# Kernel tuning notes

Hardware: AMD Instinct MI355X
Metric: run time of the kernel (lower is better)

Reference implementation:

```python
import jax, jax.numpy as jnp
import numpy as np


def _causal_kernel_mask(K):
    # casual_mask[i, K-i:] = 0 for i in 1..p
    p = K // 2
    m = np.ones((p + 1, K), np.float32)
    for i in range(1, p + 1):
        m[i, K - i:] = 0.0
    return jnp.asarray(m)


def setup_inputs() -> dict:
    rng = jax.random.key(0)
    k0, k1, k2, k3, k4 = jax.random.split(rng, 5)
    B, H, N, F = 2, 16, 1024, 64
    V, K = 32000, 5
    return {
        "input_ids": jax.random.randint(k0, (B, N), 0, V),
        "query": jax.random.normal(k1, (B, H, N, F), dtype=jnp.float32),
        "key": jax.random.normal(k2, (B, H, N, F), dtype=jnp.float32),
        "value": jax.random.normal(k3, (B, H, N, F), dtype=jnp.float32),
        "emb_weight": jax.random.normal(k4, (V, 2 * K), dtype=jnp.float32) * 0.02,
    }


def reference(input_ids, query, key, value, emb_weight):
    B, H, N, F = query.shape
    K = emb_weight.shape[1] // 2  # head/layer invariant -> emb dim = 2*K
    p = K // 2
    G = 2 * H

    # ---- get_kernel (layer 0; head_invariant + layer_invariant) ----
    kern = emb_weight[input_ids]                       # [B,N,2K]
    kern = kern.reshape(B, N, 2, 1, K)                 # [B,N,2,1,K]
    kern = jnp.broadcast_to(kern, (B, N, 2, H, K)).reshape(B, N, G, K)

    # ---- conv_key_value (for_casual=True, strict_on_casual=True) ----
    kv = jnp.concatenate([key, value], axis=1)         # [B,2H,N,F]
    kv_pad = jnp.pad(kv, ((0, 0), (0, 0), (p, p), (0, 0)))
    # unfold over token dim: [B,2H,K,N,F]
    kv_unf = jnp.stack([kv_pad[:, :, k:k + N, :] for k in range(K)], axis=2)
    cmask = _causal_kernel_mask(K)                     # [p+1,K]
    kern_m = kern[:, :, :, None, :] * cmask[None, None, None]  # [B,N,2H,p+1,K]
    # dynamic depthwise conv with per-offset causal masking
    out = jnp.einsum('bgknf,bngjk->bgjnf', kv_unf, kern_m)     # [B,2H,p+1,N,F]
    key_c = out[:, :H, 0]                              # [B,H,N,F]
    value_c = out[:, H:, 0]                            # [B,H,N,F]

    # ---- attention with causal-boundary corrections (n_past = 0) ----
    scale = 1.0 / jnp.sqrt(jnp.asarray(F, dtype=query.dtype))
    q = query * scale
    scores = jnp.einsum('bhnf,bhmf->bhnm', q, key_c)   # [B,H,N,N]

    # correct_attn_weights_near_casual_boundary
    for i in range(p):
        off = p - 1 - i
        cb_key = out[:, :H, 1 + i]                     # [B,H,N,F]
        corr = jnp.einsum('bhnf,bhnf->bhn', q[:, :, off:, :], cb_key[:, :, :N - off, :])
        rows = jnp.arange(N - off) + off
        cols = jnp.arange(N - off)
        scores = scores.at[:, :, rows, cols].set(corr)

    causal = jnp.tril(jnp.ones((N, N), dtype=bool))
    scores = jnp.where(causal, scores, jnp.asarray(-1e9, dtype=scores.dtype))
    probs = jax.nn.softmax(scores, axis=-1)
    attn = jnp.einsum('bhnm,bhmf->bhnf', probs, value_c)

    # correct_attn_output_near_casual_boundary
    for i in range(p):
        off = p - 1 - i
        cb_value = out[:, H:, 1 + i]                   # [B,H,N,F]
        idx = jnp.arange(N - off)
        diag_w = probs[:, :, idx + off, idx]           # diag offset=-off: [B,H,N-off]
        diff_v = cb_value[:, :, :N - off, :] - value_c[:, :, :N - off, :]
        diff = diag_w[..., None] * diff_v
        attn = attn + jnp.pad(diff, ((0, 0), (0, 0), (off, 0), (0, 0)))

    return attn
```

## Files before the change

kernel.cpp:

```cpp
#include <hip/hip_runtime.h>

#define HD    64
#define NSEQ  1024
#define NSLOT 40
#define CROWS 32
#define LOG2E 1.44269504088896f

typedef __attribute__((ext_vector_type(8))) __bf16 bf16x8;
typedef __attribute__((ext_vector_type(4))) float  f32x4;
typedef __attribute__((ext_vector_type(4))) unsigned short u16x4;

__device__ __constant__ unsigned char PAIRS[NSLOT] = {
    60,61,62,63, 56,57,58, 52,53,54, 48,49,50, 44,45,46,
    40,41, 36,37, 32,33, 28,29, 24, 20, 16, 12,
    59, 42, 25, 8, 55, 38, 21, 4, 51, 34, 17, 0 };

__device__ inline unsigned short f2bf(float x) {
    unsigned u = __float_as_uint(x);
    return (unsigned short)((u + 0x7fffu + ((u >> 16) & 1u)) >> 16);
}
__device__ inline unsigned pk2(float a, float b) {
    return (unsigned)f2bf(a) | ((unsigned)f2bf(b) << 16);
}
__device__ inline float bf2f(unsigned short s) {
    return __uint_as_float(((unsigned)s) << 16);
}
__device__ inline float dot4(f32x4 a, f32x4 b) {
    return a.x * b.x + a.y * b.y + a.z * b.z + a.w * b.w;
}

__global__ __launch_bounds__(256) void conv_kernel(
    const int* __restrict__ ids,
    const float* __restrict__ keyg,
    const float* __restrict__ valg,
    const float* __restrict__ qg,
    const float* __restrict__ emb,
    unsigned short* __restrict__ kc,
    unsigned short* __restrict__ vcT,
    float* __restrict__ dg1, float* __restrict__ dg2)
{
    __shared__ float se[(CROWS + 1) * 10];
    __shared__ float vtile[CROWS][68];
    int pid = blockIdx.x;
    int bh = pid & 31;
    int n0 = (pid >> 5) * CROWS;
    int b  = bh >> 4;
    int t  = threadIdx.x;
    size_t hb = (size_t)bh * NSEQ * HD;

    for (int u = t; u < (CROWS + 1) * 10; u += 256) {
        int r = u / 10, c = u - r * 10;
        int n = n0 - 1 + r;
        se[u] = (n >= 0) ? emb[(size_t)ids[b * NSEQ + n] * 10 + c] : 0.f;
    }
    __syncthreads();

    const float* kb = keyg + hb;
    const float* vb = valg + hb;
#pragma unroll
    for (int i = 0; i < 2; ++i) {
        int u  = (i << 8) + t;
        int nl = u >> 4, g4 = u & 15;
        int n  = n0 + nl, f = g4 << 2;
        const float* e  = se + (nl + 1) * 10;
        const float* ep = se + nl * 10;
        f32x4 xk[5], xv[5];
#pragma unroll
        for (int k = 0; k < 5; ++k) {
            int m = n + k - 2;
            if (m >= 0 && m < NSEQ) {
                xk[k] = *(const f32x4*)(kb + (size_t)m * HD + f);
                xv[k] = *(const f32x4*)(vb + (size_t)m * HD + f);
            } else {
                xk[k] = (f32x4){0.f, 0.f, 0.f, 0.f};
                xv[k] = (f32x4){0.f, 0.f, 0.f, 0.f};
            }
        }
        f32x4 km3 = (n >= 3) ? *(const f32x4*)(kb + (size_t)(n - 3) * HD + f)
                             : (f32x4){0.f, 0.f, 0.f, 0.f};
        f32x4 qv = *(const f32x4*)(qg + hb + (size_t)n * HD + f) * (0.125f * LOG2E);

        f32x4 k012 = e[0] * xk[0] + e[1] * xk[1] + e[2] * xk[2];
        f32x4 kcv  = k012 + e[3] * xk[3] + e[4] * xk[4];
        f32x4 vcv  = e[5] * xv[0] + e[6] * xv[1] + e[7] * xv[2] + e[8] * xv[3] + e[9] * xv[4];

        u16x4 kq;
        kq.x = f2bf(kcv.x); kq.y = f2bf(kcv.y); kq.z = f2bf(kcv.z); kq.w = f2bf(kcv.w);
        *(u16x4*)(kc + hb + (size_t)n * HD + f) = kq;
        *(f32x4*)(&vtile[nl][f]) = vcv;

        float s2 = dot4(qv, k012);
        f32x4 kj1 = ep[0] * km3 + ep[1] * xk[0] + ep[2] * xk[1] + ep[3] * xk[2];
        float s1 = dot4(qv, kj1);
#pragma unroll
        for (int o = 1; o < 16; o <<= 1) {
            s2 += __shfl_xor(s2, o, 64);
            s1 += __shfl_xor(s1, o, 64);
        }
        if (g4 == 0) {
            dg2[bh * NSEQ + n] = s2;
            dg1[bh * NSEQ + n] = s1;
        }
    }
    __syncthreads();
#pragma unroll
    for (int i = 0; i < 2; ++i) {
        int u = (i << 8) + t;
        int f = u >> 3, nn = (u & 7) << 2;
        u16x4 o;
        o.x = f2bf(vtile[nn + 0][f]);
        o.y = f2bf(vtile[nn + 1][f]);
        o.z = f2bf(vtile[nn + 2][f]);
        o.w = f2bf(vtile[nn + 3][f]);
        *(u16x4*)(vcT + ((size_t)bh * HD + f) * NSEQ + n0 + nn) = o;
    }
}

__global__ __launch_bounds__(256) void attn_kernel(
    const float* __restrict__ qg,
    const unsigned short* __restrict__ kc,
    const unsigned short* __restrict__ vcT,
    const float* __restrict__ dg1, const float* __restrict__ dg2,
    const float* __restrict__ valg, const int* __restrict__ ids,
    const float* __restrict__ emb,
    float* __restrict__ pML, unsigned short* __restrict__ pO,
    float* __restrict__ outg)
{
    __shared__ __align__(16) unsigned char sK[8192];
    __shared__ __align__(16) unsigned char sV[8192];
    __shared__ __align__(16) unsigned char sP[8192];

    int pid  = blockIdx.x;
    int bh   = pid & 31;
    int slot = pid >> 5;
    int code = PAIRS[slot];
    int j = code >> 2, cch = code & 3;
    int q0 = j << 6;
    int t0 = cch << 2;
    int len = j - (cch << 2) + 1; if (len > 4) len = 4;
    int nc  = (j >> 2) + 1;

    int t = threadIdx.x;
    int w = t >> 6, l = t & 63;
    int lq = l & 15, h = l >> 4, l7 = l & 7;
    int lid = h * 16 + lq;
    int qbw = q0 + w * 16;
    size_t hb = (size_t)bh * NSEQ * HD;

    const unsigned short* kcb = kc  + hb;
    const unsigned short* vtb = vcT + (size_t)bh * HD * NSEQ;

    bf16x8 qb0, qb1;
    {
        const float* qr = qg + hb + (size_t)(qbw + lq) * HD + 8 * h;
        f32x4 a0 = *(const f32x4*)(qr);
        f32x4 a1 = *(const f32x4*)(qr + 4);
        f32x4 b0 = *(const f32x4*)(qr + 32);
        f32x4 b1 = *(const f32x4*)(qr + 36);
        const float S = 0.125f * LOG2E;
        union { unsigned u[4]; bf16x8 v; } u0, u1;
        u0.u[0] = pk2(a0.x * S, a0.y * S); u0.u[1] = pk2(a0.z * S, a0.w * S);
        u0.u[2] = pk2(a1.x * S, a1.y * S); u0.u[3] = pk2(a1.z * S, a1.w * S);
        u1.u[0] = pk2(b0.x * S, b0.y * S); u1.u[1] = pk2(b0.z * S, b0.w * S);
        u1.u[2] = pk2(b1.x * S, b1.y * S); u1.u[3] = pk2(b1.z * S, b1.w * S);
        qb0 = u0.v; qb1 = u1.v;
    }
    float diag2_l = dg2[bh * NSEQ + qbw + lq];
    float diag1_l = dg1[bh * NSEQ + qbw + lq];

    f32x4 of[4];
#pragma unroll
    for (int ft = 0; ft < 4; ++ft) of[ft] = (f32x4){0.f, 0.f, 0.f, 0.f};
    float m_run = -1e30f, denom = 0.f;

    const int ka_off0 = ((0 + h) ^ l7) << 4;
    const int ka_off1 = ((4 + h) ^ l7) << 4;
    const int pr_base = w * 2048 + lq * 128;
    const int chk0 = ((qbw > 0 ? qbw - 1 : 0) >> 6);

    uint4 pf[4];
    auto issue = [&](int tg) {
        int kv0 = tg << 6;
#pragma unroll
        for (int i = 0; i < 4; ++i) {
            int chunk = t + (i << 8);
            int buf = chunk >> 9, loc = chunk & 511;
            int r = loc >> 3, c = loc & 7;
            int cs = c ^ (r & 7);
            pf[i] = (buf == 0)
                ? *(const uint4*)(kcb + (size_t)(kv0 + r) * HD + cs * 8)
                : *(const uint4*)(vtb + (size_t)r * NSEQ + kv0 + cs * 8);
        }
    };
    auto commit = [&]() {
#pragma unroll
        for (int i = 0; i < 4; ++i) {
            int chunk = t + (i << 8);
            int buf = chunk >> 9, loc = chunk & 511;
            int r = loc >> 3, c = loc & 7;
            *(uint4*)((buf ? sV : sK) + r * 128 + c * 16) = pf[i];
        }
    };

    issue(t0); commit();
    for (int ti = 0; ti < len; ++ti) {
        __syncthreads();
        if (ti + 1 < len) issue(t0 + ti + 1);
        int tg  = t0 + ti;
        int kv0 = tg << 6;

        f32x4 p[4];
#pragma unroll
        for (int st = 0; st < 4; ++st) {
            bf16x8 ka0 = *(const bf16x8*)(sK + st * 2048 + lq * 128 + ka_off0);
            bf16x8 ka1 = *(const bf16x8*)(sK + st * 2048 + lq * 128 + ka_off1);
            f32x4 d = (f32x4){0.f, 0.f, 0.f, 0.f};
            d = __builtin_amdgcn_mfma_f32_16x16x32_bf16(ka0, qb0, d, 0, 0, 0);
            d = __builtin_amdgcn_mfma_f32_16x16x32_bf16(ka1, qb1, d, 0, 0, 0);
            p[st] = d;
        }

        if (tg >= chk0) {
            int n_l = qbw + lq;
#pragma unroll
            for (int st = 0; st < 4; ++st)
#pragma unroll
                for (int r = 0; r < 4; ++r) {
                    int kv = kv0 + st * 16 + 4 * h + r;
                    float dd = p[st][r];
                    if (kv > n_l)           dd = -1e30f;
                    else if (kv == n_l)     dd = diag2_l;
                    else if (kv == n_l - 1) dd = diag1_l;
                    p[st][r] = dd;
                }
        }

        float tmax = -1e30f;
#pragma unroll
        for (int st = 0; st < 4; ++st)
#pragma unroll
            for (int r = 0; r < 4; ++r) tmax = fmaxf(tmax, p[st][r]);
        tmax = fmaxf(tmax, __shfl_xor(tmax, 16, 64));
        tmax = fmaxf(tmax, __shfl_xor(tmax, 32, 64));
        if (!__all(tmax <= m_run + 7.0f)) {
            float m_new = fmaxf(m_run, tmax);
            float alpha = __builtin_exp2f(m_run - m_new);
            denom *= alpha;
            m_run = m_new;
#pragma unroll
            for (int r = 0; r < 4; ++r) {
                float ar = __shfl(alpha, 4 * h + r, 64);
                of[0][r] *= ar; of[1][r] *= ar; of[2][r] *= ar; of[3][r] *= ar;
            }
        }
        float lsum = 0.f;
#pragma unroll
        for (int st = 0; st < 4; ++st)
#pragma unroll
            for (int r = 0; r < 4; ++r) {
                float e = __builtin_exp2f(p[st][r] - m_run);
                p[st][r] = e;
                lsum += e;
            }
        lsum += __shfl_xor(lsum, 16, 64);
        lsum += __shfl_xor(lsum, 32, 64);
        denom += lsum;

#pragma unroll
        for (int st = 0; st < 4; ++st) {
            uint2 uu;
            uu.x = pk2(p[st][0], p[st][1]);
            uu.y = pk2(p[st][2], p[st][3]);
            int chunk = (st << 1) + (h >> 1);
            *(uint2*)(sP + pr_base + ((chunk ^ l7) << 4) + ((h & 1) << 3)) = uu;
        }
        asm volatile("s_waitcnt lgkmcnt(0)" ::: "memory");
        __builtin_amdgcn_sched_barrier(0);

#pragma unroll
        for (int kk = 0; kk < 2; ++kk) {
            int koff = kk ? ka_off1 : ka_off0;
            bf16x8 pa = *(const bf16x8*)(sP + pr_base + koff);
#pragma unroll
            for (int ft = 0; ft < 4; ++ft) {
                bf16x8 vb = *(const bf16x8*)(sV + ft * 2048 + lq * 128 + koff);
                of[ft] = __builtin_amdgcn_mfma_f32_16x16x32_bf16(pa, vb, of[ft], 0, 0, 0);
            }
        }
        __syncthreads();
        if (ti + 1 < len) commit();
    }

    int psBase = ((bh << 4) | j) << 2;
    if (nc > 1) {
        if (h == 0) {
            float2 ml; ml.x = m_run; ml.y = denom;
            *(float2*)(pML + ((size_t)(psBase + cch) * 64 + w * 16 + lq) * 2) = ml;
        }
#pragma unroll
        for (int ft = 0; ft < 4; ++ft)
#pragma unroll
            for (int r = 0; r < 4; ++r)
                pO[(size_t)((((psBase + cch) * 4 + w) * 4 + ft) * 4 + r) * 64 + lid] =
                    f2bf(of[ft][r]);
        return;
    }

    const float* vraw = valg + hb;
    float* outr = outg + hb;
    const int* idb = ids + (size_t)(bh >> 4) * NSEQ;
#pragma unroll
    for (int r = 0; r < 4; ++r) {
        int qrow = 4 * h + r;
        int n = qbw + qrow;
        float dn = __shfl(denom,   qrow, 64);
        float mf = __shfl(m_run,   qrow, 64);
        float d2 = __shfl(diag2_l, qrow, 64);
        float d1 = __shfl(diag1_l, qrow, 64);
        float inv = 1.0f / dn;
        float p2 = __builtin_exp2f(d2 - mf) * inv;
        float p1 = (n >= 1) ? __builtin_exp2f(d1 - mf) * inv : 0.f;
        int id_n = idb[n];
        float e8  = emb[(size_t)id_n * 10 + 8];
        float e9  = emb[(size_t)id_n * 10 + 9];
        float e9p = (n >= 1) ? emb[(size_t)idb[n - 1] * 10 + 9] : 0.f;
        float ca = -(p2 * e8 + p1 * e9p);
        float cb = -p2 * e9;
#pragma unroll
        for (int ft = 0; ft < 4; ++ft) {
            int f = ft * 16 + lq;
            float v = of[ft][r] * inv;
            if (n + 1 < NSEQ) v += ca * vraw[(size_t)(n + 1) * HD + f];
            if (n + 2 < NSEQ) v += cb * vraw[(size_t)(n + 2) * HD + f];
            outr[(size_t)n * HD + f] = v;
        }
    }
}

__global__ __launch_bounds__(256) void merge_kernel(
    const float* __restrict__ pML, const unsigned short* __restrict__ pO,
    const float* __restrict__ dg1, const float* __restrict__ dg2,
    const float* __restrict__ valg, const int* __restrict__ ids,
    const float* __restrict__ emb, float* __restrict__ outg)
{
    int pid = blockIdx.x;
    int bh = pid & 31, j = (pid >> 5) + 4;
    int nc = (j >> 2) + 1;
    int t = threadIdx.x;
    int rloc = t >> 2, fg = t & 3;
    int n = (j << 6) + rloc;
    int f0 = fg << 4;
    size_t hb = (size_t)bh * NSEQ * HD;
    int psBase = ((bh << 4) | j) << 2;

    float mc[4], lc[4];
    float mg = -3e30f;
    for (int c = 0; c < nc; ++c) {
        float2 v = *(const float2*)(pML + ((size_t)(psBase + c) * 64 + rloc) * 2);
        mc[c] = v.x; lc[c] = v.y;
        mg = fmaxf(mg, mc[c]);
    }
    float D = 0.f;
    f32x4 a0 = (f32x4){0.f,0.f,0.f,0.f}, a1 = a0, a2 = a0, a3 = a0;
    for (int c = 0; c < nc; ++c) {
        float wc = __builtin_exp2f(mc[c] - mg);
        D += lc[c] * wc;
        const unsigned short* pp = pO +
            (size_t)((((psBase + c) * 4 + (rloc >> 4)) * 4 + fg) * 4 + (rloc & 3)) * 64
            + ((rloc >> 2) & 3) * 16;
        uint4 ua = *(const uint4*)(pp);
        uint4 ub = *(const uint4*)(pp + 8);
        a0.x += wc * __uint_as_float(ua.x << 16);
        a0.y += wc * __uint_as_float(ua.x & 0xffff0000u);
        a0.z += wc * __uint_as_float(ua.y << 16);
        a0.w += wc * __uint_as_float(ua.y & 0xffff0000u);
        a1.x += wc * __uint_as_float(ua.z << 16);
        a1.y += wc * __uint_as_float(ua.z & 0xffff0000u);
        a1.z += wc * __uint_as_float(ua.w << 16);
        a1.w += wc * __uint_as_float(ua.w & 0xffff0000u);
        a2.x += wc * __uint_as_float(ub.x << 16);
        a2.y += wc * __uint_as_float(ub.x & 0xffff0000u);
        a2.z += wc * __uint_as_float(ub.y << 16);
        a2.w += wc * __uint_as_float(ub.y & 0xffff0000u);
        a3.x += wc * __uint_as_float(ub.z << 16);
        a3.y += wc * __uint_as_float(ub.z & 0xffff0000u);
        a3.z += wc * __uint_as_float(ub.w << 16);
        a3.w += wc * __uint_as_float(ub.w & 0xffff0000u);
    }
    float inv = 1.0f / D;
    float d2 = dg2[bh * NSEQ + n], d1 = dg1[bh * NSEQ + n];
    float p2 = __builtin_exp2f(d2 - mg) * inv;
    float p1 = (n >= 1) ? __builtin_exp2f(d1 - mg) * inv : 0.f;
    const int* idb = ids + (size_t)(bh >> 4) * NSEQ;
    int id_n = idb[n];
    float e8  = emb[(size_t)id_n * 10 + 8];
    float e9  = emb[(size_t)id_n * 10 + 9];
    float e9p = (n >= 1) ? emb[(size_t)idb[n - 1] * 10 + 9] : 0.f;
    float ca = -(p2 * e8 + p1 * e9p);
    float cb = -p2 * e9;

    a0 *= inv; a1 *= inv; a2 *= inv; a3 *= inv;
    if (n + 1 < NSEQ) {
        const float* v1 = valg + hb + (size_t)(n + 1) * HD + f0;
        a0 += ca * *(const f32x4*)(v1);
        a1 += ca * *(const f32x4*)(v1 + 4);
        a2 += ca * *(const f32x4*)(v1 + 8);
        a3 += ca * *(const f32x4*)(v1 + 12);
    }
    if (n + 2 < NSEQ) {
        const float* v2 = valg + hb + (size_t)(n + 2) * HD + f0;
        a0 += cb * *(const f32x4*)(v2);
        a1 += cb * *(const f32x4*)(v2 + 4);
        a2 += cb * *(const f32x4*)(v2 + 8);
        a3 += cb * *(const f32x4*)(v2 + 12);
    }
    float* o = outg + hb + (size_t)n * HD + f0;
    *(f32x4*)(o)      = a0;
    *(f32x4*)(o + 4)  = a1;
    *(f32x4*)(o + 8)  = a2;
    *(f32x4*)(o + 12) = a3;
}

extern "C" void kernel_launch(void* const* d_in, const int* in_sizes, int n_in,
                              void* d_out, int out_size, void* d_ws, size_t ws_size,
                              hipStream_t stream)
{
    const int*   ids = (const int*)  d_in[0];
    const float* q   = (const float*)d_in[1];
    const float* key = (const float*)d_in[2];
    const float* val = (const float*)d_in[3];
    const float* emb = (const float*)d_in[4];
    float* out = (float*)d_out;

    char* w = (char*)d_ws;
    unsigned short* kc  = (unsigned short*)(w);
    unsigned short* vcT = (unsigned short*)(w + (4u << 20));
    float* dg1 = (float*)(w + 8388608);
    float* dg2 = (float*)(w + 8519680);
    float* pML = (float*)(w + 8650752);
    unsigned short* pO = (unsigned short*)(w + 9699328);

    conv_kernel<<<1024, 256, 0, stream>>>(ids, key, val, q, emb, kc, vcT, dg1, dg2);
    attn_kernel<<<32 * NSLOT, 256, 0, stream>>>(q, kc, vcT, dg1, dg2, val, ids, emb,
                                                pML, pO, out);
    merge_kernel<<<384, 256, 0, stream>>>(pML, pO, dg1, dg2, val, ids, emb, out);
}
```

Baseline: 60.97 us.

## Split attention blocks into single-wave blocks loading K/V directly from global

The attention kernel is relaunched with one 64-thread wavefront per block, four times as many blocks, each owning one 16-row query slice. The shared-memory K/V staging, prefetch pipeline and block-wide barriers are removed, and each wave now reads its K and transposed-V fragments directly from global memory into registers. This aims to cut barrier stalls and LDS traffic and to raise occupancy, but each wave reloads the same K/V tiles its sibling waves used to share, which increases global/L2 traffic and leaves loads without an explicit prefetch.

```diff
diff --git a/kernel.cpp b/kernel.cpp
--- a/kernel.cpp
+++ b/kernel.cpp
@@ -21,9 +21,6 @@
 }
 __device__ inline unsigned pk2(float a, float b) {
     return (unsigned)f2bf(a) | ((unsigned)f2bf(b) << 16);
-}
-__device__ inline float bf2f(unsigned short s) {
-    return __uint_as_float(((unsigned)s) << 16);
 }
 __device__ inline float dot4(f32x4 a, f32x4 b) {
     return a.x * b.x + a.y * b.y + a.z * b.z + a.w * b.w;
@@ -116,7 +113,7 @@
     }
 }
 
-__global__ __launch_bounds__(256) void attn_kernel(
+__global__ __launch_bounds__(64, 4) void attn_kernel(
     const float* __restrict__ qg,
     const unsigned short* __restrict__ kc,
     const unsigned short* __restrict__ vcT,
@@ -126,13 +123,13 @@
     float* __restrict__ pML, unsigned short* __restrict__ pO,
     float* __restrict__ outg)
 {
-    __shared__ __align__(16) unsigned char sK[8192];
-    __shared__ __align__(16) unsigned char sV[8192];
-    __shared__ __align__(16) unsigned char sP[8192];
+    __shared__ __align__(16) unsigned char sP[2048];
 
     int pid  = blockIdx.x;
     int bh   = pid & 31;
-    int slot = pid >> 5;
+    int rest = pid >> 5;
+    int w    = rest & 3;
+    int slot = rest >> 2;
     int code = PAIRS[slot];
     int j = code >> 2, cch = code & 3;
     int q0 = j << 6;
@@ -140,8 +137,7 @@
     int len = j - (cch << 2) + 1; if (len > 4) len = 4;
     int nc  = (j >> 2) + 1;
 
-    int t = threadIdx.x;
-    int w = t >> 6, l = t & 63;
+    int l = threadIdx.x & 63;
     int lq = l & 15, h = l >> 4, l7 = l & 7;
     int lid = h * 16 + lq;
     int qbw = q0 + w * 16;
@@ -173,52 +169,37 @@
     for (int ft = 0; ft < 4; ++ft) of[ft] = (f32x4){0.f, 0.f, 0.f, 0.f};
     float m_run = -1e30f, denom = 0.f;
 
-    const int ka_off0 = ((0 + h) ^ l7) << 4;
-    const int ka_off1 = ((4 + h) ^ l7) << 4;
-    const int pr_base = w * 2048 + lq * 128;
+    const int pr_base = lq * 128;
     const int chk0 = ((qbw > 0 ? qbw - 1 : 0) >> 6);
 
-    uint4 pf[4];
-    auto issue = [&](int tg) {
-        int kv0 = tg << 6;
-#pragma unroll
-        for (int i = 0; i < 4; ++i) {
-            int chunk = t + (i << 8);
-            int buf = chunk >> 9, loc = chunk & 511;
-            int r = loc >> 3, c = loc & 7;
-            int cs = c ^ (r & 7);
-            pf[i] = (buf == 0)
-                ? *(const uint4*)(kcb + (size_t)(kv0 + r) * HD + cs * 8)
-                : *(const uint4*)(vtb + (size_t)r * NSEQ + kv0 + cs * 8);
-        }
-    };
-    auto commit = [&]() {
-#pragma unroll
-        for (int i = 0; i < 4; ++i) {
-            int chunk = t + (i << 8);
-            int buf = chunk >> 9, loc = chunk & 511;
-            int r = loc >> 3, c = loc & 7;
-            *(uint4*)((buf ? sV : sK) + r * 128 + c * 16) = pf[i];
-        }
-    };
-
-    issue(t0); commit();
     for (int ti = 0; ti < len; ++ti) {
-        __syncthreads();
-        if (ti + 1 < len) issue(t0 + ti + 1);
         int tg  = t0 + ti;
         int kv0 = tg << 6;
 
+        bf16x8 ka0[4], ka1[4];
+#pragma unroll
+        for (int st = 0; st < 4; ++st) {
+            const unsigned short* kr = kcb + (size_t)(kv0 + st * 16 + lq) * HD + 8 * h;
+            ka0[st] = *(const bf16x8*)(kr);
+            ka1[st] = *(const bf16x8*)(kr + 32);
+        }
+
         f32x4 p[4];
 #pragma unroll
         for (int st = 0; st < 4; ++st) {
-            bf16x8 ka0 = *(const bf16x8*)(sK + st * 2048 + lq * 128 + ka_off0);
-            bf16x8 ka1 = *(const bf16x8*)(sK + st * 2048 + lq * 128 + ka_off1);
             f32x4 d = (f32x4){0.f, 0.f, 0.f, 0.f};
-            d = __builtin_amdgcn_mfma_f32_16x16x32_bf16(ka0, qb0, d, 0, 0, 0);
-            d = __builtin_amdgcn_mfma_f32_16x16x32_bf16(ka1, qb1, d, 0, 0, 0);
+            d = __builtin_amdgcn_mfma_f32_16x16x32_bf16(ka0[st], qb0, d, 0, 0, 0);
+            d = __builtin_amdgcn_mfma_f32_16x16x32_bf16(ka1[st], qb1, d, 0, 0, 0);
             p[st] = d;
         }
+
+        bf16x8 vbv[2][4];
+#pragma unroll
+        for (int kk = 0; kk < 2; ++kk)
+#pragma unroll
+            for (int ft = 0; ft < 4; ++ft)
+                vbv[kk][ft] = *(const bf16x8*)(
+                    vtb + (size_t)(ft * 16 + lq) * NSEQ + kv0 + 8 * (4 * kk + h));
 
         if (tg >= chk0) {
             int n_l = qbw + lq;
@@ -279,16 +260,11 @@
 
 #pragma unroll
         for (int kk = 0; kk < 2; ++kk) {
-            int koff = kk ? ka_off1 : ka_off0;
-            bf16x8 pa = *(const bf16x8*)(sP + pr_base + koff);
-#pragma unroll
-            for (int ft = 0; ft < 4; ++ft) {
-                bf16x8 vb = *(const bf16x8*)(sV + ft * 2048 + lq * 128 + koff);
-                of[ft] = __builtin_amdgcn_mfma_f32_16x16x32_bf16(pa, vb, of[ft], 0, 0, 0);
-            }
-        }
-        __syncthreads();
-        if (ti + 1 < len) commit();
+            bf16x8 pa = *(const bf16x8*)(sP + pr_base + ((((kk << 2) + h) ^ l7) << 4));
+#pragma unroll
+            for (int ft = 0; ft < 4; ++ft)
+                of[ft] = __builtin_amdgcn_mfma_f32_16x16x32_bf16(pa, vbv[kk][ft], of[ft], 0, 0, 0);
+        }
     }
 
     int psBase = ((bh << 4) | j) << 2;
@@ -441,7 +417,7 @@
     unsigned short* pO = (unsigned short*)(w + 9699328);
 
     conv_kernel<<<1024, 256, 0, stream>>>(ids, key, val, q, emb, kc, vcT, dg1, dg2);
-    attn_kernel<<<32 * NSLOT, 256, 0, stream>>>(q, kc, vcT, dg1, dg2, val, ids, emb,
-                                                pML, pO, out);
+    attn_kernel<<<32 * NSLOT * 4, 64, 0, stream>>>(q, kc, vcT, dg1, dg2, val, ids, emb,
+                                                   pML, pO, out);
     merge_kernel<<<384, 256, 0, stream>>>(pML, pO, dg1, dg2, val, ids, emb, out);
 }
```

Result: slower. 71.89 us (+17.9%).

## Pair two query blocks per 512-thread workgroup sharing K/V tiles

Applied to the files above, without the earlier changes.

The attention kernel now processes two adjacent 64-row query blocks per workgroup (8 waves, 512 threads), so each K/V tile loaded into shared memory is reused by both blocks. This halves K/V global loads per query row and the grid shrinks from 40 to 20 slots per head. Waves whose query block does not need a tile skip compute but still hit the barriers. This adds some idle-wave imbalance, doubles the P scratch in LDS, and reduces the number of workgroups available to fill the GPU.

```diff
diff --git a/kernel.cpp b/kernel.cpp
--- a/kernel.cpp
+++ b/kernel.cpp
@@ -2,7 +2,7 @@
 
 #define HD    64
 #define NSEQ  1024
-#define NSLOT 40
+#define NPB   20
 #define CROWS 32
 #define LOG2E 1.44269504088896f
 
@@ -10,10 +10,9 @@
 typedef __attribute__((ext_vector_type(4))) float  f32x4;
 typedef __attribute__((ext_vector_type(4))) unsigned short u16x4;
 
-__device__ __constant__ unsigned char PAIRS[NSLOT] = {
-    60,61,62,63, 56,57,58, 52,53,54, 48,49,50, 44,45,46,
-    40,41, 36,37, 32,33, 28,29, 24, 20, 16, 12,
-    59, 42, 25, 8, 55, 38, 21, 4, 51, 34, 17, 0 };
+__device__ __constant__ unsigned char PAIRS8[NPB] = {
+    28,29,30,31, 24,25,26, 20,21,22, 16,17, 12,13, 8, 4,
+    27, 18, 9, 0 };
 
 __device__ inline unsigned short f2bf(float x) {
     unsigned u = __float_as_uint(x);
@@ -21,9 +20,6 @@
 }
 __device__ inline unsigned pk2(float a, float b) {
     return (unsigned)f2bf(a) | ((unsigned)f2bf(b) << 16);
-}
-__device__ inline float bf2f(unsigned short s) {
-    return __uint_as_float(((unsigned)s) << 16);
 }
 __device__ inline float dot4(f32x4 a, f32x4 b) {
     return a.x * b.x + a.y * b.y + a.z * b.z + a.w * b.w;
@@ -116,7 +112,7 @@
     }
 }
 
-__global__ __launch_bounds__(256) void attn_kernel(
+__global__ __launch_bounds__(512, 4) void attn_kernel(
     const float* __restrict__ qg,
     const unsigned short* __restrict__ kc,
     const unsigned short* __restrict__ vcT,
@@ -128,23 +124,24 @@
 {
     __shared__ __align__(16) unsigned char sK[8192];
     __shared__ __align__(16) unsigned char sV[8192];
-    __shared__ __align__(16) unsigned char sP[8192];
+    __shared__ __align__(16) unsigned char sP[16384];
 
     int pid  = blockIdx.x;
     int bh   = pid & 31;
     int slot = pid >> 5;
-    int code = PAIRS[slot];
-    int j = code >> 2, cch = code & 3;
-    int q0 = j << 6;
+    int code = PAIRS8[slot];
+    int jj = code >> 2, cch = code & 3;
     int t0 = cch << 2;
-    int len = j - (cch << 2) + 1; if (len > 4) len = 4;
-    int nc  = (j >> 2) + 1;
+    int len = 2 * jj + 2 - (cch << 2); if (len > 4) len = 4;
 
     int t = threadIdx.x;
-    int w = t >> 6, l = t & 63;
+    int wv = t >> 6, l = t & 63;
+    int w_in = wv & 3;
+    int my_j = 2 * jj + (wv >> 2);
+    int nc  = (my_j >> 2) + 1;
     int lq = l & 15, h = l >> 4, l7 = l & 7;
     int lid = h * 16 + lq;
-    int qbw = q0 + w * 16;
+    int qbw = my_j * 64 + w_in * 16;
     size_t hb = (size_t)bh * NSEQ * HD;
 
     const unsigned short* kcb = kc  + hb;
@@ -175,15 +172,15 @@
 
     const int ka_off0 = ((0 + h) ^ l7) << 4;
     const int ka_off1 = ((4 + h) ^ l7) << 4;
-    const int pr_base = w * 2048 + lq * 128;
+    const int pr_base = wv * 2048 + lq * 128;
     const int chk0 = ((qbw > 0 ? qbw - 1 : 0) >> 6);
 
-    uint4 pf[4];
+    uint4 pf[2];
     auto issue = [&](int tg) {
         int kv0 = tg << 6;
 #pragma unroll
-        for (int i = 0; i < 4; ++i) {
-            int chunk = t + (i << 8);
+        for (int i = 0; i < 2; ++i) {
+            int chunk = t + (i << 9);
             int buf = chunk >> 9, loc = chunk & 511;
             int r = loc >> 3, c = loc & 7;
             int cs = c ^ (r & 7);
@@ -194,8 +191,8 @@
     };
     auto commit = [&]() {
 #pragma unroll
-        for (int i = 0; i < 4; ++i) {
-            int chunk = t + (i << 8);
+        for (int i = 0; i < 2; ++i) {
+            int chunk = t + (i << 9);
             int buf = chunk >> 9, loc = chunk & 511;
             int r = loc >> 3, c = loc & 7;
             *(uint4*)((buf ? sV : sK) + r * 128 + c * 16) = pf[i];
@@ -208,100 +205,103 @@
         if (ti + 1 < len) issue(t0 + ti + 1);
         int tg  = t0 + ti;
         int kv0 = tg << 6;
-
-        f32x4 p[4];
-#pragma unroll
-        for (int st = 0; st < 4; ++st) {
-            bf16x8 ka0 = *(const bf16x8*)(sK + st * 2048 + lq * 128 + ka_off0);
-            bf16x8 ka1 = *(const bf16x8*)(sK + st * 2048 + lq * 128 + ka_off1);
-            f32x4 d = (f32x4){0.f, 0.f, 0.f, 0.f};
-            d = __builtin_amdgcn_mfma_f32_16x16x32_bf16(ka0, qb0, d, 0, 0, 0);
-            d = __builtin_amdgcn_mfma_f32_16x16x32_bf16(ka1, qb1, d, 0, 0, 0);
-            p[st] = d;
-        }
-
-        if (tg >= chk0) {
-            int n_l = qbw + lq;
+        bool act = (tg <= my_j);
+
+        if (act) {
+            f32x4 p[4];
+#pragma unroll
+            for (int st = 0; st < 4; ++st) {
+                bf16x8 ka0 = *(const bf16x8*)(sK + st * 2048 + lq * 128 + ka_off0);
+                bf16x8 ka1 = *(const bf16x8*)(sK + st * 2048 + lq * 128 + ka_off1);
+                f32x4 d = (f32x4){0.f, 0.f, 0.f, 0.f};
+                d = __builtin_amdgcn_mfma_f32_16x16x32_bf16(ka0, qb0, d, 0, 0, 0);
+                d = __builtin_amdgcn_mfma_f32_16x16x32_bf16(ka1, qb1, d, 0, 0, 0);
+                p[st] = d;
+            }
+
+            if (tg >= chk0) {
+                int n_l = qbw + lq;
+#pragma unroll
+                for (int st = 0; st < 4; ++st)
+#pragma unroll
+                    for (int r = 0; r < 4; ++r) {
+                        int kv = kv0 + st * 16 + 4 * h + r;
+                        float dd = p[st][r];
+                        if (kv > n_l)           dd = -1e30f;
+                        else if (kv == n_l)     dd = diag2_l;
+                        else if (kv == n_l - 1) dd = diag1_l;
+                        p[st][r] = dd;
+                    }
+            }
+
+            float tmax = -1e30f;
 #pragma unroll
             for (int st = 0; st < 4; ++st)
 #pragma unroll
+                for (int r = 0; r < 4; ++r) tmax = fmaxf(tmax, p[st][r]);
+            tmax = fmaxf(tmax, __shfl_xor(tmax, 16, 64));
+            tmax = fmaxf(tmax, __shfl_xor(tmax, 32, 64));
+            if (!__all(tmax <= m_run + 7.0f)) {
+                float m_new = fmaxf(m_run, tmax);
+                float alpha = __builtin_exp2f(m_run - m_new);
+                denom *= alpha;
+                m_run = m_new;
+#pragma unroll
                 for (int r = 0; r < 4; ++r) {
-                    int kv = kv0 + st * 16 + 4 * h + r;
-                    float dd = p[st][r];
-                    if (kv > n_l)           dd = -1e30f;
-                    else if (kv == n_l)     dd = diag2_l;
-                    else if (kv == n_l - 1) dd = diag1_l;
-                    p[st][r] = dd;
+                    float ar = __shfl(alpha, 4 * h + r, 64);
+                    of[0][r] *= ar; of[1][r] *= ar; of[2][r] *= ar; of[3][r] *= ar;
                 }
-        }
-
-        float tmax = -1e30f;
-#pragma unroll
-        for (int st = 0; st < 4; ++st)
-#pragma unroll
-            for (int r = 0; r < 4; ++r) tmax = fmaxf(tmax, p[st][r]);
-        tmax = fmaxf(tmax, __shfl_xor(tmax, 16, 64));
-        tmax = fmaxf(tmax, __shfl_xor(tmax, 32, 64));
-        if (!__all(tmax <= m_run + 7.0f)) {
-            float m_new = fmaxf(m_run, tmax);
-            float alpha = __builtin_exp2f(m_run - m_new);
-            denom *= alpha;
-            m_run = m_new;
-#pragma unroll
-            for (int r = 0; r < 4; ++r) {
-                float ar = __shfl(alpha, 4 * h + r, 64);
-                of[0][r] *= ar; of[1][r] *= ar; of[2][r] *= ar; of[3][r] *= ar;
-            }
-        }
-        float lsum = 0.f;
-#pragma unroll
-        for (int st = 0; st < 4; ++st)
-#pragma unroll
-            for (int r = 0; r < 4; ++r) {
-                float e = __builtin_exp2f(p[st][r] - m_run);
-                p[st][r] = e;
-                lsum += e;
-            }
-        lsum += __shfl_xor(lsum, 16, 64);
-        lsum += __shfl_xor(lsum, 32, 64);
-        denom += lsum;
-
-#pragma unroll
-        for (int st = 0; st < 4; ++st) {
-            uint2 uu;
-            uu.x = pk2(p[st][0], p[st][1]);
-            uu.y = pk2(p[st][2], p[st][3]);
-            int chunk = (st << 1) + (h >> 1);
-            *(uint2*)(sP + pr_base + ((chunk ^ l7) << 4) + ((h & 1) << 3)) = uu;
-        }
-        asm volatile("s_waitcnt lgkmcnt(0)" ::: "memory");
-        __builtin_amdgcn_sched_barrier(0);
-
-#pragma unroll
-        for (int kk = 0; kk < 2; ++kk) {
-            int koff = kk ? ka_off1 : ka_off0;
-            bf16x8 pa = *(const bf16x8*)(sP + pr_base + koff);
-#pragma unroll
-            for (int ft = 0; ft < 4; ++ft) {
-                bf16x8 vb = *(const bf16x8*)(sV + ft * 2048 + lq * 128 + koff);
-                of[ft] = __builtin_amdgcn_mfma_f32_16x16x32_bf16(pa, vb, of[ft], 0, 0, 0);
+            }
+            float lsum = 0.f;
+#pragma unroll
+            for (int st = 0; st < 4; ++st)
+#pragma unroll
+                for (int r = 0; r < 4; ++r) {
+                    float e = __builtin_exp2f(p[st][r] - m_run);
+                    p[st][r] = e;
+                    lsum += e;
+                }
+            lsum += __shfl_xor(lsum, 16, 64);
+            lsum += __shfl_xor(lsum, 32, 64);
+            denom += lsum;
+
+#pragma unroll
+            for (int st = 0; st < 4; ++st) {
+                uint2 uu;
+                uu.x = pk2(p[st][0], p[st][1]);
+                uu.y = pk2(p[st][2], p[st][3]);
+                int chunk = (st << 1) + (h >> 1);
+                *(uint2*)(sP + pr_base + ((chunk ^ l7) << 4) + ((h & 1) << 3)) = uu;
+            }
+            asm volatile("s_waitcnt lgkmcnt(0)" ::: "memory");
+            __builtin_amdgcn_sched_barrier(0);
+
+#pragma unroll
+            for (int kk = 0; kk < 2; ++kk) {
+                int koff = kk ? ka_off1 : ka_off0;
+                bf16x8 pa = *(const bf16x8*)(sP + pr_base + koff);
+#pragma unroll
+                for (int ft = 0; ft < 4; ++ft) {
+                    bf16x8 vb = *(const bf16x8*)(sV + ft * 2048 + lq * 128 + koff);
+                    of[ft] = __builtin_amdgcn_mfma_f32_16x16x32_bf16(pa, vb, of[ft], 0, 0, 0);
+                }
             }
         }
         __syncthreads();
         if (ti + 1 < len) commit();
     }
 
-    int psBase = ((bh << 4) | j) << 2;
+    int psBase = ((bh << 4) | my_j) << 2;
     if (nc > 1) {
         if (h == 0) {
             float2 ml; ml.x = m_run; ml.y = denom;
-            *(float2*)(pML + ((size_t)(psBase + cch) * 64 + w * 16 + lq) * 2) = ml;
+            *(float2*)(pML + ((size_t)(psBase + cch) * 64 + w_in * 16 + lq) * 2) = ml;
         }
 #pragma unroll
         for (int ft = 0; ft < 4; ++ft)
 #pragma unroll
             for (int r = 0; r < 4; ++r)
-                pO[(size_t)((((psBase + cch) * 4 + w) * 4 + ft) * 4 + r) * 64 + lid] =
+                pO[(size_t)((((psBase + cch) * 4 + w_in) * 4 + ft) * 4 + r) * 64 + lid] =
                     f2bf(of[ft][r]);
         return;
     }
@@ -441,7 +441,7 @@
     unsigned short* pO = (unsigned short*)(w + 9699328);
 
     conv_kernel<<<1024, 256, 0, stream>>>(ids, key, val, q, emb, kc, vcT, dg1, dg2);
-    attn_kernel<<<32 * NSLOT, 256, 0, stream>>>(q, kc, vcT, dg1, dg2, val, ids, emb,
-                                                pML, pO, out);
+    attn_kernel<<<32 * NPB, 512, 0, stream>>>(q, kc, vcT, dg1, dg2, val, ids, emb,
+                                              pML, pO, out);
     merge_kernel<<<384, 256, 0, stream>>>(pML, pO, dg1, dg2, val, ids, emb, out);
 }
```

Result: faster. 56.90 us (-6.7%).
